# Kernel tuning notes

Measured on AMD Instinct MI355X. Metric: run time of the kernel, lower is better.

The kernel has to match this reference:

```python
import jax, jax.numpy as jnp
import numpy as np

B, T, D_IN = 2, 2048, 1024
H, D_HEAD = 16, 64
D_INNER = H * D_HEAD  # 1024
D_OUT = D_HEAD        # out_proj maps d_inner -> d_out


def setup_inputs() -> dict:
    key = jax.random.key(0)
    ks = jax.random.split(key, 6)
    s_in = 1.0 / np.sqrt(D_IN)
    s_inner = 1.0 / np.sqrt(D_INNER)
    return {
        "x": jax.random.normal(ks[0], (B, T, D_IN), dtype=jnp.float32),
        "Wq": jax.random.uniform(ks[1], (D_IN, D_INNER), jnp.float32, -s_in, s_in),
        "Wk": jax.random.uniform(ks[2], (D_IN, D_INNER), jnp.float32, -s_in, s_in),
        "Wv": jax.random.uniform(ks[3], (D_IN, D_INNER), jnp.float32, -s_in, s_in),
        "Wo": jax.random.uniform(ks[4], (D_INNER, D_OUT), jnp.float32, -s_inner, s_inner),
        "bo": jax.random.uniform(ks[5], (D_OUT,), jnp.float32, -s_inner, s_inner),
    }


def reference(x, Wq, Wk, Wv, Wo, bo):
    b, t, _ = x.shape
    # projections -> [b, h, t, d]
    def split_heads(y):
        return y.reshape(b, t, H, D_HEAD).transpose(0, 2, 1, 3)
    q = split_heads(x @ Wq)
    k = split_heads(x @ Wk)
    v = split_heads(x @ Wv)
    scores = jnp.einsum("bhqd,bhkd->bhqk", q, k)
    causal = jnp.triu(jnp.ones((t, t), dtype=bool), k=1)
    scores = jnp.where(causal, -jnp.inf, scores)
    # NOTE: original scales by sqrt(d_out*num_heads), not sqrt(head_dim)
    attn = jax.nn.softmax(scores / np.sqrt(D_INNER), axis=-1)
    y = jnp.einsum("bhqk,bhkd->bhqd", attn, v)
    y = y.transpose(0, 2, 1, 3).reshape(b, t, D_INNER)
    return y @ Wo + bo
```

## Files before the change

### kernel.cpp

```cpp
#include <hip/hip_runtime.h>
#include <hip/hip_bf16.h>

typedef __attribute__((ext_vector_type(8))) short short8;
typedef __attribute__((ext_vector_type(4))) float f32x4;
typedef __attribute__((ext_vector_type(8))) unsigned short ushort8v;


__device__ __forceinline__ unsigned short f2bf(float f) {
  union { float f; unsigned int u; } x; x.f = f;
  unsigned int r = x.u + 0x7FFFu + ((x.u >> 16) & 1u);
  return (unsigned short)(r >> 16);
}

__device__ __forceinline__ unsigned int pk_bf16(float a, float b) {
  __hip_bfloat162 h = __float22bfloat162_rn(float2{a, b});
  union { __hip_bfloat162 h; unsigned int u; } c; c.h = h;
  return c.u;
}

__device__ __forceinline__ void gload_lds16(const void* g, void* l) {
  __builtin_amdgcn_global_load_lds(
      (const __attribute__((address_space(1))) void*)g,
      (__attribute__((address_space(3))) void*)l, 16, 0, 0);
}


__global__ __launch_bounds__(256) void prep(
    const float* __restrict__ x,
    const float* __restrict__ Wq, const float* __restrict__ Wk, const float* __restrict__ Wv,
    const float* __restrict__ Wo, const float* __restrict__ bo,
    unsigned short* __restrict__ xb,
    unsigned short* __restrict__ wqt, unsigned short* __restrict__ wkt,
    unsigned short* __restrict__ wvt, unsigned short* __restrict__ wot,
    float* __restrict__ out) {
  __shared__ float tile[32][33];
  int b = blockIdx.x;
  if (b < 4096) {
    int i = (b * 256 + threadIdx.x) * 4;
    float4 f = *(const float4*)(x + i);
    uint2 o; o.x = pk_bf16(f.x, f.y); o.y = pk_bf16(f.z, f.w);
    *(uint2*)(xb + i) = o;
  } else if (b < 7168) {
    int idx = b - 4096;
    int z = idx >> 10, rem = idx & 1023;
    const float* src = (z == 0) ? Wq : (z == 1) ? Wk : Wv;
    unsigned short* dst = (z == 0) ? wqt : (z == 1) ? wkt : wvt;
    int kx = (rem & 31) * 32, ny = (rem >> 5) * 32;
    int tx = threadIdx.x & 31, ty = threadIdx.x >> 5;
    #pragma unroll
    for (int r = 0; r < 32; r += 8)
      tile[ty + r][tx] = src[(size_t)(kx + ty + r) * 1024 + ny + tx];
    __syncthreads();
    #pragma unroll
    for (int r = 0; r < 32; r += 8)
      dst[(size_t)(ny + ty + r) * 1024 + kx + tx] = f2bf(tile[tx][ty + r]);
  } else if (b < 7232) {
    int idx = b - 7168;
    int kx = (idx & 31) * 32, ny = (idx >> 5) * 32;
    int tx = threadIdx.x & 31, ty = threadIdx.x >> 5;
    #pragma unroll
    for (int r = 0; r < 32; r += 8)
      tile[ty + r][tx] = Wo[(size_t)(kx + ty + r) * 64 + ny + tx];
    __syncthreads();
    #pragma unroll
    for (int r = 0; r < 32; r += 8)
      wot[(size_t)(ny + ty + r) * 1024 + kx + tx] = f2bf(tile[tx][ty + r]);
  } else {
    int t = (b - 7232) * 256 + threadIdx.x;
    float4 bi = *(const float4*)(bo + (t & 15) * 4);
    *(float4*)(out + (size_t)t * 4) = bi;
  }
}


__global__ __launch_bounds__(256) void qkv_gemm(
    const unsigned short* __restrict__ Xb,
    const unsigned short* __restrict__ Wqt, const unsigned short* __restrict__ Wkt,
    const unsigned short* __restrict__ Wvt,
    unsigned short* __restrict__ Oq, unsigned short* __restrict__ Ok,
    unsigned short* __restrict__ Ovt) {
  constexpr int Kd = 1024;
  __shared__ __align__(16) unsigned short As[128 * 64];
  __shared__ __align__(16) unsigned short Bs[128 * 64];
  int z = blockIdx.z;
  int m0, n0;
  const unsigned short *Arow, *Brow;
  if (z == 2) {
    m0 = blockIdx.x * 128; n0 = blockIdx.y * 128;
    Arow = Xb; Brow = Wvt;
  } else {
    m0 = blockIdx.y * 128; n0 = blockIdx.x * 128;
    Arow = (z == 0) ? Wqt : Wkt; Brow = Xb;
  }
  int tid = threadIdx.x, lane = tid & 63, wave = tid >> 6;
  int wm = wave >> 1, wn = wave & 1;
  int l15 = lane & 15, quad = lane >> 4;
  int swz = l15 & 7;

  f32x4 acc[4][4] = {};

  for (int k0 = 0; k0 < Kd; k0 += 64) {
    __syncthreads();
    #pragma unroll
    for (int r = 0; r < 4; ++r) {
      int i = tid + 256 * r;
      int row = i >> 3, c8 = i & 7;
      int gc8 = c8 ^ (row & 7);
      gload_lds16(Arow + (size_t)(m0 + row) * Kd + k0 + gc8 * 8, &As[i * 8]);
    }
    #pragma unroll
    for (int r = 0; r < 4; ++r) {
      int i = tid + 256 * r;
      int row = i >> 3, c8 = i & 7;
      int gc8 = c8 ^ (row & 7);
      gload_lds16(Brow + (size_t)(n0 + row) * Kd + k0 + gc8 * 8, &Bs[i * 8]);
    }
    __syncthreads();
    short8 af[4][2], bf[4][2];
    #pragma unroll
    for (int s = 0; s < 2; ++s) {
      #pragma unroll
      for (int i = 0; i < 4; ++i)
        af[i][s] = *(const short8*)&As[(wm * 64 + i * 16 + l15) * 64 + (((s << 2) + quad) ^ swz) * 8];
      #pragma unroll
      for (int j = 0; j < 4; ++j)
        bf[j][s] = *(const short8*)&Bs[(wn * 64 + j * 16 + l15) * 64 + (((s << 2) + quad) ^ swz) * 8];
    }
    #pragma unroll
    for (int s = 0; s < 2; ++s)
      #pragma unroll
      for (int i = 0; i < 4; ++i)
        #pragma unroll
        for (int j = 0; j < 4; ++j)
          acc[i][j] = __builtin_amdgcn_mfma_f32_16x16x32_bf16(af[i][s], bf[j][s], acc[i][j], 0, 0, 0);
  }

  if (z == 2) {
    #pragma unroll
    for (int i = 0; i < 4; ++i) {
      int tbase = m0 + wm * 64 + i * 16 + quad * 4;
      int b = tbase >> 11, tt = tbase & 2047;
      #pragma unroll
      for (int j = 0; j < 4; ++j) {
        int dm = n0 + wn * 64 + j * 16 + l15;
        int h = dm >> 6, d = dm & 63;
        uint2 pk;
        pk.x = pk_bf16(acc[i][j][0], acc[i][j][1]);
        pk.y = pk_bf16(acc[i][j][2], acc[i][j][3]);
        *(uint2*)(Ovt + (((size_t)(b * 16 + h) * 64 + d) << 11) + tt) = pk;
      }
    }
  } else {
    unsigned short* O = (z == 0) ? Oq : Ok;
    float scale = (z == 0) ? 0.03125f : 1.0f;
    #pragma unroll
    for (int i = 0; i < 4; ++i) {
      int dmbase = m0 + wm * 64 + i * 16 + quad * 4;
      int h = dmbase >> 6, d0 = dmbase & 63;
      #pragma unroll
      for (int j = 0; j < 4; ++j) {
        int t = n0 + wn * 64 + j * 16 + l15;
        int b = t >> 11, tt = t & 2047;
        uint2 pk;
        pk.x = pk_bf16(acc[i][j][0] * scale, acc[i][j][1] * scale);
        pk.y = pk_bf16(acc[i][j][2] * scale, acc[i][j][3] * scale);
        *(uint2*)(O + (((size_t)(b * 16 + h) * 2048 + tt) << 6) + d0) = pk;
      }
    }
  }
}


__global__ __launch_bounds__(256, 2) void attn10(
    const unsigned short* __restrict__ Qg, const unsigned short* __restrict__ Kg,
    const unsigned short* __restrict__ Vtg, unsigned short* __restrict__ Yg) {
  constexpr int T = 2048;
  __shared__ __align__(16) unsigned short Ks[64 * 72];
  __shared__ __align__(16) unsigned short Vs[64 * 72];
  __shared__ __align__(16) unsigned short Ps[4][32 * 72];
  int bh = blockIdx.x;
  int by = blockIdx.y;
  int pp = (by < 8) ? by : 23 - by;
  int qtA = pp, qtB = 31 - pp;
  int tid = threadIdx.x, lane = tid & 63, wave = tid >> 6;
  int l15 = lane & 15, quad = lane >> 4;
  const unsigned short* Qb = Qg + (size_t)bh * T * 64;
  const unsigned short* Kb = Kg + (size_t)bh * T * 64;
  const unsigned short* Vb = Vtg + (size_t)bh * 64 * T;
  int h = bh & 15, b = bh >> 4;
  int qw[2] = {qtA * 64 + wave * 16, qtB * 64 + wave * 16};

  short8 qf[2][2];
  #pragma unroll
  for (int jq = 0; jq < 2; ++jq)
    #pragma unroll
    for (int s = 0; s < 2; ++s)
      qf[jq][s] = *(const short8*)(Qb + (size_t)(qw[jq] + l15) * 64 + quad * 8 + 32 * s);

  f32x4 Oacc[2][4] = {};
  float m_run[2] = {-__builtin_inff(), -__builtin_inff()};
  float l_run[2] = {0.f, 0.f};

  ushort8v kpre[2], vpre[2];
  #pragma unroll
  for (int r = 0; r < 2; ++r) {
    int i = tid + 256 * r;
    kpre[r] = *(const ushort8v*)(Kb + (size_t)(i >> 3) * 64 + (i & 7) * 8);
    vpre[r] = *(const ushort8v*)(Vb + (size_t)(i >> 3) * T + (i & 7) * 8);
  }

  for (int kt = 0; kt <= qtA; ++kt) {
    __syncthreads();
    #pragma unroll
    for (int r = 0; r < 2; ++r) {
      int i = tid + 256 * r;
      *(ushort8v*)&Ks[(i >> 3) * 72 + (i & 7) * 8] = kpre[r];
      *(ushort8v*)&Vs[(i >> 3) * 72 + (i & 7) * 8] = vpre[r];
    }
    __syncthreads();
    {
      #pragma unroll
      for (int r = 0; r < 2; ++r) {
        int i = tid + 256 * r;
        kpre[r] = *(const ushort8v*)(Kb + (size_t)((kt + 1) * 64 + (i >> 3)) * 64 + (i & 7) * 8);
        vpre[r] = *(const ushort8v*)(Vb + (size_t)(i >> 3) * T + (kt + 1) * 64 + (i & 7) * 8);
      }
    }

    f32x4 S[4][2] = {};
    #pragma unroll
    for (int s = 0; s < 2; ++s)
      #pragma unroll
      for (int mi = 0; mi < 4; ++mi) {
        short8 kf = *(const short8*)&Ks[(mi * 16 + l15) * 72 + quad * 8 + 32 * s];
        #pragma unroll
        for (int jq = 0; jq < 2; ++jq)
          S[mi][jq] = __builtin_amdgcn_mfma_f32_16x16x32_bf16(kf, qf[jq][s], S[mi][jq], 0, 0, 0);
      }

    if (kt == qtA) {
      int ql = wave * 16 + l15;
      #pragma unroll
      for (int mi = 0; mi < 4; ++mi) {
        int tokl = mi * 16 + quad * 4;
        #pragma unroll
        for (int r = 0; r < 4; ++r)
          if (tokl + r > ql) S[mi][0][r] = -__builtin_inff();
      }
    }

    float alpha[2];
    #pragma unroll
    for (int jq = 0; jq < 2; ++jq) {
      float vmax = -__builtin_inff();
      #pragma unroll
      for (int mi = 0; mi < 4; ++mi)
        #pragma unroll
        for (int r = 0; r < 4; ++r)
          vmax = fmaxf(vmax, S[mi][jq][r]);
      vmax = fmaxf(vmax, __shfl_xor(vmax, 16));
      vmax = fmaxf(vmax, __shfl_xor(vmax, 32));
      float mnew = fmaxf(m_run[jq], vmax);
      alpha[jq] = __expf(m_run[jq] - mnew);
      m_run[jq] = mnew;
      float rs = 0.f;
      #pragma unroll
      for (int mi = 0; mi < 4; ++mi) {
        float p0 = __expf(S[mi][jq][0] - mnew);
        float p1 = __expf(S[mi][jq][1] - mnew);
        float p2 = __expf(S[mi][jq][2] - mnew);
        float p3 = __expf(S[mi][jq][3] - mnew);
        rs += (p0 + p1) + (p2 + p3);
        uint2 pk;
        pk.x = pk_bf16(p0, p1);
        pk.y = pk_bf16(p2, p3);
        *(uint2*)&Ps[wave][(jq * 16 + l15) * 72 + mi * 16 + quad * 4] = pk;
      }
      rs += __shfl_xor(rs, 16);
      rs += __shfl_xor(rs, 32);
      l_run[jq] = l_run[jq] * alpha[jq] + rs;
    }

    #pragma unroll
    for (int jq = 0; jq < 2; ++jq)
      #pragma unroll
      for (int jd = 0; jd < 4; ++jd)
        #pragma unroll
        for (int r = 0; r < 4; ++r)
          Oacc[jq][jd][r] *= alpha[jq];

    #pragma unroll
    for (int s = 0; s < 2; ++s) {
      short8 vfr[4];
      #pragma unroll
      for (int jd = 0; jd < 4; ++jd)
        vfr[jd] = *(const short8*)&Vs[(jd * 16 + l15) * 72 + s * 32 + quad * 8];
      #pragma unroll
      for (int jq = 0; jq < 2; ++jq) {
        short8 pf = *(const short8*)&Ps[wave][(jq * 16 + l15) * 72 + s * 32 + quad * 8];
        #pragma unroll
        for (int jd = 0; jd < 4; ++jd)
          Oacc[jq][jd] = __builtin_amdgcn_mfma_f32_16x16x32_bf16(vfr[jd], pf, Oacc[jq][jd], 0, 0, 0);
      }
    }
  }

  for (int kt = qtA + 1; kt <= qtB; ++kt) {
    __syncthreads();
    #pragma unroll
    for (int r = 0; r < 2; ++r) {
      int i = tid + 256 * r;
      *(ushort8v*)&Ks[(i >> 3) * 72 + (i & 7) * 8] = kpre[r];
      *(ushort8v*)&Vs[(i >> 3) * 72 + (i & 7) * 8] = vpre[r];
    }
    __syncthreads();
    if (kt < qtB) {
      #pragma unroll
      for (int r = 0; r < 2; ++r) {
        int i = tid + 256 * r;
        kpre[r] = *(const ushort8v*)(Kb + (size_t)((kt + 1) * 64 + (i >> 3)) * 64 + (i & 7) * 8);
        vpre[r] = *(const ushort8v*)(Vb + (size_t)(i >> 3) * T + (kt + 1) * 64 + (i & 7) * 8);
      }
    }

    f32x4 S[4] = {};
    #pragma unroll
    for (int s = 0; s < 2; ++s)
      #pragma unroll
      for (int mi = 0; mi < 4; ++mi) {
        short8 kf = *(const short8*)&Ks[(mi * 16 + l15) * 72 + quad * 8 + 32 * s];
        S[mi] = __builtin_amdgcn_mfma_f32_16x16x32_bf16(kf, qf[1][s], S[mi], 0, 0, 0);
      }

    if (kt == qtB) {
      int ql = wave * 16 + l15;
      #pragma unroll
      for (int mi = 0; mi < 4; ++mi) {
        int tokl = mi * 16 + quad * 4;
        #pragma unroll
        for (int r = 0; r < 4; ++r)
          if (tokl + r > ql) S[mi][r] = -__builtin_inff();
      }
    }

    float vmax = -__builtin_inff();
    #pragma unroll
    for (int mi = 0; mi < 4; ++mi)
      #pragma unroll
      for (int r = 0; r < 4; ++r)
        vmax = fmaxf(vmax, S[mi][r]);
    vmax = fmaxf(vmax, __shfl_xor(vmax, 16));
    vmax = fmaxf(vmax, __shfl_xor(vmax, 32));
    float mnew = fmaxf(m_run[1], vmax);
    float alpha = __expf(m_run[1] - mnew);
    m_run[1] = mnew;
    float rs = 0.f;
    #pragma unroll
    for (int mi = 0; mi < 4; ++mi) {
      float p0 = __expf(S[mi][0] - mnew);
      float p1 = __expf(S[mi][1] - mnew);
      float p2 = __expf(S[mi][2] - mnew);
      float p3 = __expf(S[mi][3] - mnew);
      rs += (p0 + p1) + (p2 + p3);
      uint2 pk;
      pk.x = pk_bf16(p0, p1);
      pk.y = pk_bf16(p2, p3);
      *(uint2*)&Ps[wave][(16 + l15) * 72 + mi * 16 + quad * 4] = pk;
    }
    rs += __shfl_xor(rs, 16);
    rs += __shfl_xor(rs, 32);
    l_run[1] = l_run[1] * alpha + rs;

    #pragma unroll
    for (int jd = 0; jd < 4; ++jd)
      #pragma unroll
      for (int r = 0; r < 4; ++r)
        Oacc[1][jd][r] *= alpha;

    #pragma unroll
    for (int s = 0; s < 2; ++s) {
      short8 pf = *(const short8*)&Ps[wave][(16 + l15) * 72 + s * 32 + quad * 8];
      #pragma unroll
      for (int jd = 0; jd < 4; ++jd) {
        short8 vfr = *(const short8*)&Vs[(jd * 16 + l15) * 72 + s * 32 + quad * 8];
        Oacc[1][jd] = __builtin_amdgcn_mfma_f32_16x16x32_bf16(vfr, pf, Oacc[1][jd], 0, 0, 0);
      }
    }
  }

  #pragma unroll
  for (int jq = 0; jq < 2; ++jq) {
    float linv = 1.f / l_run[jq];
    int q = qw[jq] + l15;
    size_t row = (size_t)(b * 2048 + q) * 1024 + h * 64 + quad * 4;
    #pragma unroll
    for (int jd = 0; jd < 4; ++jd) {
      uint2 pk;
      pk.x = pk_bf16(Oacc[jq][jd][0] * linv, Oacc[jq][jd][1] * linv);
      pk.y = pk_bf16(Oacc[jq][jd][2] * linv, Oacc[jq][jd][3] * linv);
      *(uint2*)(Yg + row + jd * 16) = pk;
    }
  }
}


__global__ __launch_bounds__(256) void oproj(
    const unsigned short* __restrict__ Y, const unsigned short* __restrict__ Wot,
    float* __restrict__ out) {
  __shared__ __align__(16) unsigned short As[64 * 32];
  __shared__ __align__(16) unsigned short Bs[64 * 32];
  int m0 = blockIdx.x * 64;
  int kbase = blockIdx.y * 256;
  int tid = threadIdx.x, lane = tid & 63, wave = tid >> 6;
  int l15 = lane & 15, quad = lane >> 4;
  f32x4 acc[4] = {};
  for (int k0 = kbase; k0 < kbase + 256; k0 += 32) {
    __syncthreads();
    {
      int row = tid >> 2, c8 = (tid & 3) * 8;
      gload_lds16(Y + (size_t)(m0 + row) * 1024 + k0 + c8, &As[tid * 8]);
      gload_lds16(Wot + (size_t)row * 1024 + k0 + c8, &Bs[tid * 8]);
    }
    __syncthreads();
    short8 af = *(const short8*)&As[(wave * 16 + l15) * 32 + quad * 8];
    #pragma unroll
    for (int j = 0; j < 4; ++j) {
      short8 bf = *(const short8*)&Bs[(j * 16 + l15) * 32 + quad * 8];
      acc[j] = __builtin_amdgcn_mfma_f32_16x16x32_bf16(af, bf, acc[j], 0, 0, 0);
    }
  }
  #pragma unroll
  for (int j = 0; j < 4; ++j) {
    int n = j * 16 + l15;
    #pragma unroll
    for (int r = 0; r < 4; ++r) {
      int m = m0 + wave * 16 + quad * 4 + r;
      atomicAdd(&out[(size_t)m * 64 + n], acc[j][r]);
    }
  }
}


extern "C" void kernel_launch(void* const* d_in, const int* in_sizes, int n_in,
                              void* d_out, int out_size, void* d_ws, size_t ws_size,
                              hipStream_t stream) {
  const float* x  = (const float*)d_in[0];
  const float* Wq = (const float*)d_in[1];
  const float* Wk = (const float*)d_in[2];
  const float* Wv = (const float*)d_in[3];
  const float* Wo = (const float*)d_in[4];
  const float* bo = (const float*)d_in[5];
  float* out = (float*)d_out;
  char* ws = (char*)d_ws;

  unsigned short* xb  = (unsigned short*)(ws);
  unsigned short* wqt = (unsigned short*)(ws + (8ull << 20));
  unsigned short* wkt = (unsigned short*)(ws + (10ull << 20));
  unsigned short* wvt = (unsigned short*)(ws + (12ull << 20));
  unsigned short* wot = (unsigned short*)(ws + (14ull << 20));
  unsigned short* q   = (unsigned short*)(ws + (15ull << 20));
  unsigned short* k   = (unsigned short*)(ws + (23ull << 20));
  unsigned short* vt  = (unsigned short*)(ws + (31ull << 20));
  unsigned short* y   = (unsigned short*)(ws + (39ull << 20));

  prep<<<7488, 256, 0, stream>>>(x, Wq, Wk, Wv, Wo, bo, xb, wqt, wkt, wvt, wot, out);
  qkv_gemm<<<dim3(32, 8, 3), 256, 0, stream>>>(xb, wqt, wkt, wvt, q, k, vt);
  attn10<<<dim3(32, 16), 256, 0, stream>>>(q, k, vt, y);
  oproj<<<dim3(64, 4), 256, 0, stream>>>(y, wot, out);
}
```

Measured before the change: 162.1 us.

## Fuse output projection into attention epilogue with per-head atomic accumulation

The attention kernel now stages its normalized bf16 output tile in shared memory and multiplies it by the head's 64x64 slice of the transposed output weight with MFMA, then atomically adds the result into the fp32 output. This removes the separate oproj launch and the round trip of the bf16 Y tensor through global memory. In exchange every head issues float atomics to the same output rows (16-way contention per element), and each wave loads its own copy of the weight slice from global memory.

Measured after the change: 195.3 us. +20.5%, slower.

```diff
diff --git a/kernel.cpp b/kernel.cpp
--- a/kernel.cpp
+++ b/kernel.cpp
@@ -171,9 +171,10 @@
 }
 
 
-__global__ __launch_bounds__(256, 2) void attn10(
+__global__ __launch_bounds__(256, 2) void attn11(
     const unsigned short* __restrict__ Qg, const unsigned short* __restrict__ Kg,
-    const unsigned short* __restrict__ Vtg, unsigned short* __restrict__ Yg) {
+    const unsigned short* __restrict__ Vtg, const unsigned short* __restrict__ Wot,
+    float* __restrict__ out) {
   constexpr int T = 2048;
   __shared__ __align__(16) unsigned short Ks[64 * 72];
   __shared__ __align__(16) unsigned short Vs[64 * 72];
@@ -391,51 +392,42 @@
   #pragma unroll
   for (int jq = 0; jq < 2; ++jq) {
     float linv = 1.f / l_run[jq];
-    int q = qw[jq] + l15;
-    size_t row = (size_t)(b * 2048 + q) * 1024 + h * 64 + quad * 4;
     #pragma unroll
     for (int jd = 0; jd < 4; ++jd) {
       uint2 pk;
       pk.x = pk_bf16(Oacc[jq][jd][0] * linv, Oacc[jq][jd][1] * linv);
       pk.y = pk_bf16(Oacc[jq][jd][2] * linv, Oacc[jq][jd][3] * linv);
-      *(uint2*)(Yg + row + jd * 16) = pk;
-    }
-  }
-}
-
-
-__global__ __launch_bounds__(256) void oproj(
-    const unsigned short* __restrict__ Y, const unsigned short* __restrict__ Wot,
-    float* __restrict__ out) {
-  __shared__ __align__(16) unsigned short As[64 * 32];
-  __shared__ __align__(16) unsigned short Bs[64 * 32];
-  int m0 = blockIdx.x * 64;
-  int kbase = blockIdx.y * 256;
-  int tid = threadIdx.x, lane = tid & 63, wave = tid >> 6;
-  int l15 = lane & 15, quad = lane >> 4;
-  f32x4 acc[4] = {};
-  for (int k0 = kbase; k0 < kbase + 256; k0 += 32) {
-    __syncthreads();
-    {
-      int row = tid >> 2, c8 = (tid & 3) * 8;
-      gload_lds16(Y + (size_t)(m0 + row) * 1024 + k0 + c8, &As[tid * 8]);
-      gload_lds16(Wot + (size_t)row * 1024 + k0 + c8, &Bs[tid * 8]);
-    }
-    __syncthreads();
-    short8 af = *(const short8*)&As[(wave * 16 + l15) * 32 + quad * 8];
-    #pragma unroll
-    for (int j = 0; j < 4; ++j) {
-      short8 bf = *(const short8*)&Bs[(j * 16 + l15) * 32 + quad * 8];
-      acc[j] = __builtin_amdgcn_mfma_f32_16x16x32_bf16(af, bf, acc[j], 0, 0, 0);
-    }
-  }
-  #pragma unroll
-  for (int j = 0; j < 4; ++j) {
-    int n = j * 16 + l15;
-    #pragma unroll
-    for (int r = 0; r < 4; ++r) {
-      int m = m0 + wave * 16 + quad * 4 + r;
-      atomicAdd(&out[(size_t)m * 64 + n], acc[j][r]);
+      *(uint2*)&Ps[wave][(jq * 16 + l15) * 72 + jd * 16 + quad * 4] = pk;
+    }
+  }
+  short8 wf[4][2];
+  #pragma unroll
+  for (int mi = 0; mi < 4; ++mi)
+    #pragma unroll
+    for (int s = 0; s < 2; ++s)
+      wf[mi][s] = *(const short8*)(Wot + (size_t)(mi * 16 + l15) * 1024 + h * 64 + s * 32 + quad * 8);
+
+  f32x4 op[4][2] = {};
+  #pragma unroll
+  for (int s = 0; s < 2; ++s)
+    #pragma unroll
+    for (int jq = 0; jq < 2; ++jq) {
+      short8 pf = *(const short8*)&Ps[wave][(jq * 16 + l15) * 72 + s * 32 + quad * 8];
+      #pragma unroll
+      for (int mi = 0; mi < 4; ++mi)
+        op[mi][jq] = __builtin_amdgcn_mfma_f32_16x16x32_bf16(wf[mi][s], pf, op[mi][jq], 0, 0, 0);
+    }
+
+  #pragma unroll
+  for (int jq = 0; jq < 2; ++jq) {
+    int q = qw[jq] + l15;
+    float* orow = out + (size_t)(b * 2048 + q) * 64;
+    #pragma unroll
+    for (int mi = 0; mi < 4; ++mi) {
+      int dout = mi * 16 + quad * 4;
+      #pragma unroll
+      for (int r = 0; r < 4; ++r)
+        atomicAdd(orow + dout + r, op[mi][jq][r]);
     }
   }
 }
@@ -461,10 +453,8 @@
   unsigned short* q   = (unsigned short*)(ws + (15ull << 20));
   unsigned short* k   = (unsigned short*)(ws + (23ull << 20));
   unsigned short* vt  = (unsigned short*)(ws + (31ull << 20));
-  unsigned short* y   = (unsigned short*)(ws + (39ull << 20));
 
   prep<<<7488, 256, 0, stream>>>(x, Wq, Wk, Wv, Wo, bo, xb, wqt, wkt, wvt, wot, out);
   qkv_gemm<<<dim3(32, 8, 3), 256, 0, stream>>>(xb, wqt, wkt, wvt, q, k, vt);
-  attn10<<<dim3(32, 16), 256, 0, stream>>>(q, k, vt, y);
-  oproj<<<dim3(64, 4), 256, 0, stream>>>(y, wot, out);
-}
+  attn11<<<dim3(32, 16), 256, 0, stream>>>(q, k, vt, wot, out);
+}
```
